# Performance work log

Hardware: AMD Instinct MI355X
Metric: run time of the kernel (lower is better)

## Reference

```python
import jax, jax.numpy as jnp
import numpy as np

B, IN, H, Z = 2048, 1024, 1024, 256


def setup_inputs() -> dict:
    key = jax.random.key(0)
    ks = jax.random.split(key, 17)
    s = 1.0 / np.sqrt(H)  # matches reset_parameters uniform(-stdv, stdv)
    u = lambda k, shape: jax.random.uniform(k, shape, minval=-s, maxval=s, dtype=jnp.float32)
    return {
        'src_x': jax.random.normal(ks[0], (B, IN), dtype=jnp.float32),
        'h': jax.random.normal(ks[1], (B, H), dtype=jnp.float32),
        'c': jax.random.normal(ks[2], (B, H), dtype=jnp.float32),
        'src_meta': jax.random.normal(ks[3], (B, Z), dtype=jnp.float32),
        'zh_w': u(ks[4], (4 * Z, Z)),
        'zh_b': u(ks[5], (4 * Z,)),
        'zx_w': u(ks[6], (4 * Z, Z)),
        'zx_b': u(ks[7], (4 * Z,)),
        'zb_w': u(ks[8], (4 * Z, Z)),
        'dh_w': u(ks[9], (4, H, Z)),
        'dx_w': u(ks[10], (4, H, Z)),
        'db_w': u(ks[11], (4, H, Z)),
        'db_b': u(ks[12], (4, H)),
        'w_h': u(ks[13], (4, H, H)),
        'w_x': u(ks[14], (4, H, IN)),
        'ln_w': u(ks[15], (4, H)),
        'ln_b': u(ks[16], (4, H)),
    }


def reference(src_x, h, c, src_meta, zh_w, zh_b, zx_w, zx_b, zb_w,
              dh_w, dx_w, db_w, db_b, w_h, w_x, ln_w, ln_b):
    b = src_x.shape[0]
    # hypernetwork projections, reshaped to [B, 4 gates, Z]
    zh = (src_meta @ zh_w.T + zh_b).reshape(b, 4, -1)
    zx = (src_meta @ zx_w.T + zx_b).reshape(b, 4, -1)
    zb = (src_meta @ zb_w.T).reshape(b, 4, -1)
    # per-gate scaling vectors d_h, d_x and bias d_b: [B, 4, H]
    d_h = jnp.einsum('bgz,ghz->bgh', zh, dh_w)
    d_x = jnp.einsum('bgz,ghz->bgh', zx, dx_w)
    d_b = jnp.einsum('bgz,ghz->bgh', zb, db_w) + db_b[None]
    # main LSTM matmuls: [B, 4, H]
    wh = jnp.einsum('ghj,bj->bgh', w_h, h)
    wx = jnp.einsum('ghj,bj->bgh', w_x, src_x)
    y = d_h * wh + d_x * wx + d_b
    # per-gate LayerNorm over hidden dim (eps = 1e-5, torch default)
    mu = jnp.mean(y, axis=-1, keepdims=True)
    var = jnp.var(y, axis=-1, keepdims=True)
    yn = (y - mu) * jax.lax.rsqrt(var + 1e-5) * ln_w[None] + ln_b[None]
    i, f, g, o = yn[:, 0], yn[:, 1], yn[:, 2], yn[:, 3]
    c_next = jax.nn.sigmoid(f) * c + jax.nn.sigmoid(i) * jnp.tanh(g)
    h_next = jax.nn.sigmoid(o) * jnp.tanh(c_next)
    return (h_next, c_next)
```

## Files before the change

### kernel.cpp

```cpp
#include <hip/hip_runtime.h>

typedef __attribute__((ext_vector_type(4))) float f32x4;
typedef __attribute__((ext_vector_type(16))) float f32x16;
typedef __attribute__((ext_vector_type(8))) short bf16x8;

#define DEVFN static __device__ __forceinline__

DEVFN unsigned short f2bf(float f) {
  union { float f; unsigned u; } x; x.f = f;
  unsigned r = x.u + 0x7fffu + ((x.u >> 16) & 1u);
  return (unsigned short)(r >> 16);
}
DEVFN float bf2f(unsigned short u) {
  union { unsigned u; float f; } x; x.u = ((unsigned)u) << 16;
  return x.f;
}

DEVFN void gload_lds16(const unsigned short* g, unsigned short* l) {
  __builtin_amdgcn_global_load_lds(
      (const __attribute__((address_space(1))) unsigned int*)g,
      (__attribute__((address_space(3))) unsigned int*)l, 16, 0, 0);
}

#define NSEG 8
struct SegTable {
  const float* src[NSEG];
  unsigned short* dst[NSEG];
  int chunks[NSEG];
};

__global__ __launch_bounds__(256) void cast_f32_bf16(SegTable st) {
  int c = blockIdx.x;
  int s = 0;
  while (c >= st.chunks[s]) { c -= st.chunks[s]; ++s; }
  const float* src = st.src[s] + (long)c * 4096;
  unsigned short* dst = st.dst[s] + (long)c * 4096;
  const int t = threadIdx.x;
#pragma unroll
  for (int i = 0; i < 4; ++i) {
    float4 v = *(const float4*)(src + t * 4 + i * 1024);
    ushort4 o;
    o.x = f2bf(v.x); o.y = f2bf(v.y); o.z = f2bf(v.z); o.w = f2bf(v.w);
    *(ushort4*)(dst + t * 4 + i * 1024) = o;
  }
}

__global__ __launch_bounds__(256) void tcast_z(
    const float* __restrict__ zh_w, const float* __restrict__ zx_w,
    const float* __restrict__ zb_w, unsigned short* __restrict__ WzT) {
  const int zz = blockIdx.z;
  const int t = zz >> 2, g = zz & 3;
  const float* src =
      (t == 0 ? zh_w : (t == 1 ? zx_w : zb_w)) + (long)g * 65536;
  unsigned short* dst = WzT + (long)zz * 65536;
  const int j0 = blockIdx.x * 64, k0 = blockIdx.y * 64;
  __shared__ float T[64][65];
  const int tid = threadIdx.x;
  const int jr = tid >> 2, kc = (tid & 3) * 16;
#pragma unroll
  for (int i = 0; i < 4; ++i) {
    float4 v = *(const float4*)(src + (long)(j0 + jr) * 256 + k0 + kc + i * 4);
    T[jr][kc + i * 4 + 0] = v.x;
    T[jr][kc + i * 4 + 1] = v.y;
    T[jr][kc + i * 4 + 2] = v.z;
    T[jr][kc + i * 4 + 3] = v.w;
  }
  __syncthreads();
  const int kr = tid >> 2, jc = (tid & 3) * 16;
  unsigned short tmp[16];
#pragma unroll
  for (int i = 0; i < 16; ++i) tmp[i] = f2bf(T[jc + i][kr]);
  *(bf16x8*)(dst + (long)(k0 + kr) * 256 + j0 + jc) = *(bf16x8*)&tmp[0];
  *(bf16x8*)(dst + (long)(k0 + kr) * 256 + j0 + jc + 8) = *(bf16x8*)&tmp[8];
}

__global__ __launch_bounds__(256) void fbias_kernel(
    const float* __restrict__ zh_b, const float* __restrict__ zx_b,
    const float* __restrict__ db_b, const float* __restrict__ dh_w,
    const float* __restrict__ dx_w, float* __restrict__ F) {
  if (blockIdx.x >= 128) {
    const int idx = (blockIdx.x - 128) * 1024 + threadIdx.x * 4;
    *(float4*)(F + 8192 + idx) = *(const float4*)(db_b + idx);
    return;
  }
  const int wgid = blockIdx.x * 4 + (threadIdx.x >> 6);
  const int lane = threadIdx.x & 63;
  const int t = wgid >> 8, g = (wgid >> 6) & 3, hbase = (wgid & 63) * 16;
  const float* zb = (t == 0 ? zh_b : zx_b) + g * 256;
  const float* dw = (t == 0 ? dh_w : dx_w) + (long)g * 262144;
  float4 zv = *(const float4*)(zb + lane * 4);
#pragma unroll
  for (int i = 0; i < 16; ++i) {
    const int h = hbase + i;
    float4 wv = *(const float4*)(dw + (long)h * 256 + lane * 4);
    float s = zv.x * wv.x + zv.y * wv.y + zv.z * wv.z + zv.w * wv.w;
#pragma unroll
    for (int off = 32; off; off >>= 1) s += __shfl_down(s, off);
    if (lane == 0) F[(t * 4 + g) * 1024 + h] = s;
  }
}

DEVFN void gemm128_body(const unsigned short* __restrict__ A,
                        const unsigned short* __restrict__ W,
                        unsigned short* __restrict__ C,
                        const float* __restrict__ bias,
                        int lda, int ldb, int ldc, int K,
                        int bx, int by,
                        unsigned short* As, unsigned short* Bs) {
  const int m0 = by * 128, n0 = bx * 128;
  const int tid = threadIdx.x;
  const int lane = tid & 63, wid = tid >> 6;
  const int wr = wid >> 1, wc = wid & 1;

  const int srow = tid >> 2, scol = (tid & 3) * 8;
  const unsigned short* Ag0 = A + (long)(m0 + srow) * lda + scol;
  const unsigned short* Ag1 = A + (long)(m0 + 64 + srow) * lda + scol;
  const unsigned short* Wg0 = W + (long)(n0 + srow) * ldb + scol;
  const unsigned short* Wg1 = W + (long)(n0 + 64 + srow) * ldb + scol;
  unsigned short* As0 = &As[tid * 8];
  unsigned short* As1 = &As[2048 + tid * 8];
  unsigned short* Bs0 = &Bs[tid * 8];
  unsigned short* Bs1 = &Bs[2048 + tid * 8];

  const int r = lane & 15, q = lane >> 4;

  f32x4 acc[4][4];
#pragma unroll
  for (int m = 0; m < 4; ++m)
#pragma unroll
    for (int n = 0; n < 4; ++n) acc[m][n] = (f32x4)0.f;

  for (int k0 = 0; k0 < K; k0 += 32) {
    gload_lds16(Ag0 + k0, As0);
    gload_lds16(Ag1 + k0, As1);
    gload_lds16(Wg0 + k0, Bs0);
    gload_lds16(Wg1 + k0, Bs1);
    __syncthreads();

    bf16x8 af[4], bfr[4];
#pragma unroll
    for (int m = 0; m < 4; ++m)
      af[m] = *(const bf16x8*)&As[(wr * 64 + m * 16 + r) * 32 + q * 8];
#pragma unroll
    for (int n = 0; n < 4; ++n)
      bfr[n] = *(const bf16x8*)&Bs[(wc * 64 + n * 16 + r) * 32 + q * 8];
#pragma unroll
    for (int m = 0; m < 4; ++m)
#pragma unroll
      for (int n = 0; n < 4; ++n)
        acc[m][n] = __builtin_amdgcn_mfma_f32_16x16x32_bf16(af[m], bfr[n],
                                                            acc[m][n], 0, 0, 0);
    __syncthreads();
  }

#pragma unroll
  for (int m = 0; m < 4; ++m) {
    const int row = m0 + wr * 64 + m * 16 + q * 4;
#pragma unroll
    for (int n = 0; n < 4; ++n) {
      const int col = n0 + wc * 64 + n * 16 + r;
      float bv = bias ? bias[col] : 0.f;
#pragma unroll
      for (int j = 0; j < 4; ++j) {
        float v = acc[m][n][j] + bv;
        C[(long)(row + j) * ldc + col] = f2bf(v);
      }
    }
  }
}

__global__ __launch_bounds__(256) void gemm_e(
    const unsigned short* __restrict__ Wd, const unsigned short* __restrict__ WzT,
    unsigned short* __restrict__ E) {
  __shared__ __align__(16) unsigned short As[4096];
  __shared__ __align__(16) unsigned short Bs[4096];
  const int zz = blockIdx.z;
  gemm128_body(Wd + (long)zz * 262144, WzT + (long)zz * 65536,
               E + (long)zz * 262144, nullptr,
               256, 256, 256, 256, blockIdx.x, blockIdx.y, As, Bs);
}

__global__ __launch_bounds__(256) void gemm_y(
    const unsigned short* __restrict__ meta_bf,
    const unsigned short* __restrict__ E,
    const unsigned short* __restrict__ whx,
    const float* __restrict__ F,
    unsigned short* __restrict__ Y) {
  __shared__ __align__(16) unsigned short As[4096];
  __shared__ __align__(16) unsigned short Bs[4096];
  const int g = blockIdx.z;
  const int m0 = blockIdx.y * 128, n0 = blockIdx.x * 128;
  const int tid = threadIdx.x;
  const int lane = tid & 63, wid = tid >> 6;
  const int wr = wid >> 1, wc = wid & 1;
  const int r = lane & 15, q = lane >> 4;
  const int srow = tid >> 2, scol = (tid & 3) * 8;

  const unsigned short* Ag0 = meta_bf + (long)(m0 + srow) * 256 + scol;
  const unsigned short* Ag1 = meta_bf + (long)(m0 + 64 + srow) * 256 + scol;
  unsigned short* As0 = &As[tid * 8];
  unsigned short* As1 = &As[2048 + tid * 8];
  unsigned short* Bs0 = &Bs[tid * 8];
  unsigned short* Bs1 = &Bs[2048 + tid * 8];

  f32x4 yacc[4][4];
#pragma unroll
  for (int m = 0; m < 4; ++m)
#pragma unroll
    for (int n = 0; n < 4; ++n) yacc[m][n] = (f32x4)0.f;

#pragma unroll 1
  for (int t = 0; t < 3; ++t) {
    const unsigned short* W = E + ((long)(t * 4 + g)) * 262144;
    const unsigned short* Wg0 = W + (long)(n0 + srow) * 256 + scol;
    const unsigned short* Wg1 = W + (long)(n0 + 64 + srow) * 256 + scol;

    f32x4 acc[4][4];
#pragma unroll
    for (int m = 0; m < 4; ++m)
#pragma unroll
      for (int n = 0; n < 4; ++n) acc[m][n] = (f32x4)0.f;

    for (int k0 = 0; k0 < 256; k0 += 32) {
      gload_lds16(Ag0 + k0, As0);
      gload_lds16(Ag1 + k0, As1);
      gload_lds16(Wg0 + k0, Bs0);
      gload_lds16(Wg1 + k0, Bs1);
      __syncthreads();

      bf16x8 af[4], bfr[4];
#pragma unroll
      for (int m = 0; m < 4; ++m)
        af[m] = *(const bf16x8*)&As[(wr * 64 + m * 16 + r) * 32 + q * 8];
#pragma unroll
      for (int n = 0; n < 4; ++n)
        bfr[n] = *(const bf16x8*)&Bs[(wc * 64 + n * 16 + r) * 32 + q * 8];
#pragma unroll
      for (int m = 0; m < 4; ++m)
#pragma unroll
        for (int n = 0; n < 4; ++n)
          acc[m][n] = __builtin_amdgcn_mfma_f32_16x16x32_bf16(
              af[m], bfr[n], acc[m][n], 0, 0, 0);
      __syncthreads();
    }

    if (t < 2) {
      const unsigned short* wsrc = whx + (long)t * 8388608;
#pragma unroll
      for (int n = 0; n < 4; ++n) {
        const int cl = wc * 64 + n * 16 + r;
        const float fv = F[(t * 4 + g) * 1024 + n0 + cl];
        const long colg = (long)g * 1024 + n0 + cl;
#pragma unroll
        for (int m = 0; m < 4; ++m) {
          const int row = m0 + wr * 64 + m * 16 + q * 4;
#pragma unroll
          for (int j = 0; j < 4; ++j) {
            const float wv = bf2f(wsrc[(long)(row + j) * 4096 + colg]);
            yacc[m][n][j] += (acc[m][n][j] + fv) * wv;
          }
        }
      }
    } else {
#pragma unroll
      for (int n = 0; n < 4; ++n) {
        const int cl = wc * 64 + n * 16 + r;
        const float fv = F[(8 + g) * 1024 + n0 + cl];
#pragma unroll
        for (int m = 0; m < 4; ++m)
#pragma unroll
          for (int j = 0; j < 4; ++j)
            yacc[m][n][j] += acc[m][n][j] + fv;
      }
    }
  }

#pragma unroll
  for (int m = 0; m < 4; ++m) {
    const int row = m0 + wr * 64 + m * 16 + q * 4;
#pragma unroll
    for (int n = 0; n < 4; ++n) {
      const long colg = (long)g * 1024 + n0 + wc * 64 + n * 16 + r;
#pragma unroll
      for (int j = 0; j < 4; ++j)
        Y[(long)(row + j) * 4096 + colg] = f2bf(yacc[m][n][j]);
    }
  }
}

__global__ __launch_bounds__(512, 2) void gemm256_whx(
    const unsigned short* __restrict__ Aall,
    const unsigned short* __restrict__ Ball,
    unsigned short* __restrict__ Call) {
  __shared__ __align__(16) unsigned short As[2][2][8192];
  __shared__ __align__(16) unsigned short Bs[2][2][8192];

  const int bid = blockIdx.x;
  const int swz = (bid & 7) * 32 + (bid >> 3);
  const int z = swz >> 7;
  const int rr = swz & 127;
  const int sb = rr >> 5, wq = rr & 31;
  const int my = (sb & 1) * 4 + (wq >> 3);
  const int nx = (sb >> 1) * 8 + (wq & 7);

  const unsigned short* Ag = Aall + (long)z * 2097152 + (long)my * 262144;
  const unsigned short* Bg = Ball + (long)z * 4194304 + (long)nx * 262144;
  unsigned short* Cg = Call + (long)z * 8388608 + (long)my * 1048576 + nx * 256;

  const int tid = threadIdx.x;
  const int lane = tid & 63, wid = tid >> 6;
  const int wm = wid >> 2, wn = wid & 3;
  const int l31 = lane & 31, l5 = lane >> 5;
  const int sw = l31 & 7;

  const int srow = tid >> 3, sslot = tid & 7;
  const int gcol = (sslot ^ (srow & 7)) * 8;
  const unsigned short* AgS = Ag + (long)srow * 1024 + gcol;
  const unsigned short* BgS = Bg + (long)srow * 1024 + gcol;

  auto stageA = [&](int buf, int half, int kt) {
    const unsigned short* s = AgS + half * 131072 + kt * 64;
    unsigned short* d = &As[buf][half][tid * 8];
    gload_lds16(s, d);
    gload_lds16(s + 65536, d + 4096);
  };
  auto stageB = [&](int buf, int half, int kt) {
    const unsigned short* s = BgS + half * 131072 + kt * 64;
    unsigned short* d = &Bs[buf][half][tid * 8];
    gload_lds16(s, d);
    gload_lds16(s + 65536, d + 4096);
  };

  int koff[4];
#pragma unroll
  for (int ks = 0; ks < 4; ++ks) koff[ks] = ((ks * 2 + l5) ^ sw) * 8;

  const int bhalf = wn >> 1;
  int brow[2];
#pragma unroll
  for (int nt = 0; nt < 2; ++nt) brow[nt] = ((wn & 1) * 64 + nt * 32 + l31) * 64;
  int arow[4];
#pragma unroll
  for (int mt = 0; mt < 4; ++mt) arow[mt] = (mt * 32 + l31) * 64;

  f32x16 acc[4][2];
#pragma unroll
  for (int m = 0; m < 4; ++m)
#pragma unroll
    for (int n = 0; n < 2; ++n) acc[m][n] = (f32x16)0.f;

  stageA(0, 0, 0); stageB(0, 0, 0); stageA(0, 1, 0); stageB(0, 1, 0);
  stageA(1, 0, 1); stageB(1, 0, 1);
  asm volatile("s_waitcnt vmcnt(4)" ::: "memory");
  __builtin_amdgcn_s_barrier();

#pragma unroll 2
  for (int T = 0; T < 16; ++T) {
    const int buf = T & 1, nb = buf ^ 1;

    if (T < 15) { stageA(nb, 1, T + 1); stageB(nb, 1, T + 1); }

    bf16x8 bfg[2][4], af[2][4];
    const unsigned short* Ab = &As[buf][wm][0];
    {
      const unsigned short* Bb = &Bs[buf][bhalf][0];
#pragma unroll
      for (int nt = 0; nt < 2; ++nt)
#pragma unroll
        for (int ks = 0; ks < 4; ++ks)
          bfg[nt][ks] = *(const bf16x8*)(Bb + brow[nt] + koff[ks]);
#pragma unroll
      for (int m2 = 0; m2 < 2; ++m2)
#pragma unroll
        for (int ks = 0; ks < 4; ++ks)
          af[m2][ks] = *(const bf16x8*)(Ab + arow[m2] + koff[ks]);
    }

    __builtin_amdgcn_s_setprio(1);
#pragma unroll
    for (int m2 = 0; m2 < 2; ++m2)
#pragma unroll
      for (int nt = 0; nt < 2; ++nt)
#pragma unroll
        for (int ks = 0; ks < 4; ++ks)
          acc[m2][nt] = __builtin_amdgcn_mfma_f32_32x32x16_bf16(
              af[m2][ks], bfg[nt][ks], acc[m2][nt], 0, 0, 0);
    __builtin_amdgcn_s_setprio(0);

#pragma unroll
    for (int m2 = 0; m2 < 2; ++m2)
#pragma unroll
      for (int ks = 0; ks < 4; ++ks)
        af[m2][ks] = *(const bf16x8*)(Ab + arow[2 + m2] + koff[ks]);

    asm volatile("s_waitcnt lgkmcnt(0)" ::: "memory");
    __builtin_amdgcn_sched_barrier(0);
    __builtin_amdgcn_s_barrier();

    if (T < 14) { stageA(buf, 0, T + 2); stageB(buf, 0, T + 2); }

    __builtin_amdgcn_s_setprio(1);
#pragma unroll
    for (int m2 = 0; m2 < 2; ++m2)
#pragma unroll
      for (int nt = 0; nt < 2; ++nt)
#pragma unroll
        for (int ks = 0; ks < 4; ++ks)
          acc[2 + m2][nt] = __builtin_amdgcn_mfma_f32_32x32x16_bf16(
              af[m2][ks], bfg[nt][ks], acc[2 + m2][nt], 0, 0, 0);
    __builtin_amdgcn_s_setprio(0);

    if (T < 14) {
      asm volatile("s_waitcnt vmcnt(4)" ::: "memory");
      __builtin_amdgcn_s_barrier();
    } else if (T == 14) {
      asm volatile("s_waitcnt vmcnt(0)" ::: "memory");
      __builtin_amdgcn_s_barrier();
    }
  }

#pragma unroll
  for (int mt = 0; mt < 4; ++mt) {
#pragma unroll
    for (int nt = 0; nt < 2; ++nt) {
      const int rb = wm * 128 + mt * 32 + 4 * l5;
      const int cb = wn * 64 + nt * 32 + l31;
#pragma unroll
      for (int reg = 0; reg < 16; ++reg) {
        const int row = rb + (reg & 3) + 8 * (reg >> 2);
        Cg[(long)row * 4096 + cb] = f2bf(acc[mt][nt][reg]);
      }
    }
  }
}

DEVFN void ld4bf(const unsigned short* p, float* o) {
  ushort4 v = *(const ushort4*)p;
  o[0] = bf2f(v.x); o[1] = bf2f(v.y); o[2] = bf2f(v.z); o[3] = bf2f(v.w);
}

__global__ __launch_bounds__(256) void epilogue2(
    const unsigned short* __restrict__ Y,
    const float* __restrict__ c_in,
    const float* __restrict__ ln_w, const float* __restrict__ ln_b,
    float* __restrict__ out) {
  const long b = blockIdx.x;
  const int t = threadIdx.x;
  const int lane = t & 63, wid = t >> 6;

  __shared__ float redS[4][4], redQ[4][4];
  float y[4][4];

#pragma unroll
  for (int g = 0; g < 4; ++g) {
    ld4bf(Y + b * 4096 + g * 1024 + t * 4, y[g]);
    float s = 0.f, sq = 0.f;
#pragma unroll
    for (int j = 0; j < 4; ++j) { s += y[g][j]; sq += y[g][j] * y[g][j]; }
#pragma unroll
    for (int off = 32; off; off >>= 1) {
      s += __shfl_down(s, off);
      sq += __shfl_down(sq, off);
    }
    if (lane == 0) { redS[g][wid] = s; redQ[g][wid] = sq; }
  }
  __syncthreads();

  float yn[4][4];
#pragma unroll
  for (int g = 0; g < 4; ++g) {
    float S = redS[g][0] + redS[g][1] + redS[g][2] + redS[g][3];
    float SQ = redQ[g][0] + redQ[g][1] + redQ[g][2] + redQ[g][3];
    float mu = S * (1.f / 1024.f);
    float var = SQ * (1.f / 1024.f) - mu * mu;
    float rs = rsqrtf(var + 1e-5f);
    const int base = g * 1024 + t * 4;
    float4 lw = *(const float4*)(ln_w + base);
    float4 lb = *(const float4*)(ln_b + base);
    yn[g][0] = (y[g][0] - mu) * rs * lw.x + lb.x;
    yn[g][1] = (y[g][1] - mu) * rs * lw.y + lb.y;
    yn[g][2] = (y[g][2] - mu) * rs * lw.z + lb.z;
    yn[g][3] = (y[g][3] - mu) * rs * lw.w + lb.w;
  }

  float4 cp = *(const float4*)(c_in + b * 1024 + t * 4);
  float cin[4] = {cp.x, cp.y, cp.z, cp.w};
  float hn[4], cn[4];
#pragma unroll
  for (int j = 0; j < 4; ++j) {
    float ii = yn[0][j], ff = yn[1][j], gg = yn[2][j], oo = yn[3][j];
    float si = 1.f / (1.f + expf(-ii));
    float sf = 1.f / (1.f + expf(-ff));
    float so = 1.f / (1.f + expf(-oo));
    float cnj = sf * cin[j] + si * tanhf(gg);
    cn[j] = cnj;
    hn[j] = so * tanhf(cnj);
  }
  float4 ho = {hn[0], hn[1], hn[2], hn[3]};
  float4 co = {cn[0], cn[1], cn[2], cn[3]};
  *(float4*)(out + b * 1024 + t * 4) = ho;
  *(float4*)(out + 2097152L + b * 1024 + t * 4) = co;
}

extern "C" void kernel_launch(void* const* d_in, const int* in_sizes, int n_in,
                              void* d_out, int out_size, void* d_ws,
                              size_t ws_size, hipStream_t stream) {
  const float* src_x = (const float*)d_in[0];
  const float* h_in  = (const float*)d_in[1];
  const float* c_in  = (const float*)d_in[2];
  const float* meta  = (const float*)d_in[3];
  const float* zh_w  = (const float*)d_in[4];
  const float* zh_b  = (const float*)d_in[5];
  const float* zx_w  = (const float*)d_in[6];
  const float* zx_b  = (const float*)d_in[7];
  const float* zb_w  = (const float*)d_in[8];
  const float* dh_w  = (const float*)d_in[9];
  const float* dx_w  = (const float*)d_in[10];
  const float* db_w  = (const float*)d_in[11];
  const float* db_b  = (const float*)d_in[12];
  const float* w_h   = (const float*)d_in[13];
  const float* w_x   = (const float*)d_in[14];
  const float* ln_w  = (const float*)d_in[15];
  const float* ln_b  = (const float*)d_in[16];

  char* ws = (char*)d_ws;
  unsigned short* h_bf    = (unsigned short*)(ws + 0);
  unsigned short* x_bf    = (unsigned short*)(ws + 4194304);
  unsigned short* meta_bf = (unsigned short*)(ws + 8388608);
  unsigned short* Wh      = (unsigned short*)(ws + 9437184);
  unsigned short* Wx      = (unsigned short*)(ws + 17825792);
  unsigned short* Wd      = (unsigned short*)(ws + 26214400);
  unsigned short* WzT     = (unsigned short*)(ws + 32505856);
  unsigned short* E       = (unsigned short*)(ws + 34078720);
  float*          F       = (float*)(ws + 40370176);
  unsigned short* Ybuf    = (unsigned short*)(ws + 40419328);
  unsigned short* whx     = (unsigned short*)(ws + 57196544);
  if (ws_size < 90750976) return;

  SegTable st;
  int i = 0, total = 0;
  auto add = [&](const float* s, unsigned short* d, int n) {
    st.src[i] = s; st.dst[i] = d; st.chunks[i] = n / 4096;
    total += n / 4096; ++i;
  };
  add(h_in, h_bf, 2048 * 1024);
  add(src_x, x_bf, 2048 * 1024);
  add(meta, meta_bf, 2048 * 256);
  add(w_h, Wh, 4096 * 1024);
  add(w_x, Wx, 4096 * 1024);
  add(dh_w, Wd, 4 * 1024 * 256);
  add(dx_w, Wd + 1048576, 4 * 1024 * 256);
  add(db_w, Wd + 2097152, 4 * 1024 * 256);
  cast_f32_bf16<<<total, 256, 0, stream>>>(st);

  tcast_z<<<dim3(4, 4, 12), 256, 0, stream>>>(zh_w, zx_w, zb_w, WzT);
  fbias_kernel<<<132, 256, 0, stream>>>(zh_b, zx_b, db_b, dh_w, dx_w, F);

  gemm_e<<<dim3(2, 8, 12), 256, 0, stream>>>(Wd, WzT, E);

  gemm256_whx<<<256, 512, 0, stream>>>(h_bf, Wh, whx);

  gemm_y<<<dim3(8, 16, 4), 256, 0, stream>>>(meta_bf, E, whx, F, Ybuf);

  epilogue2<<<2048, 256, 0, stream>>>(Ybuf, c_in, ln_w, ln_b, (float*)d_out);
}
```

Before: 128.3 us.

## Merge prep kernels and stage gemm_y epilogue through LDS for coalesced access

Folds the three preprocessing kernels (cast, transpose-cast, bias) into one launch that dispatches on block index, removing two kernel launches. In gemm_y, each gate accumulator is biased, packed to bf16 and written to an enlarged shared buffer. Threads then re-read it in row-major 8-wide vectors, so the whx reads and final Y stores become coalesced 16-byte accesses instead of scattered 2-byte ones. This costs extra syncthreads, more LDS per block and an extra bf16 rounding of the intermediate before multiplying.

```diff
diff --git a/kernel.cpp b/kernel.cpp
--- a/kernel.cpp
+++ b/kernel.cpp
@@ -29,62 +29,67 @@
   int chunks[NSEG];
 };
 
-__global__ __launch_bounds__(256) void cast_f32_bf16(SegTable st) {
-  int c = blockIdx.x;
-  int s = 0;
-  while (c >= st.chunks[s]) { c -= st.chunks[s]; ++s; }
-  const float* src = st.src[s] + (long)c * 4096;
-  unsigned short* dst = st.dst[s] + (long)c * 4096;
-  const int t = threadIdx.x;
-#pragma unroll
-  for (int i = 0; i < 4; ++i) {
-    float4 v = *(const float4*)(src + t * 4 + i * 1024);
-    ushort4 o;
-    o.x = f2bf(v.x); o.y = f2bf(v.y); o.z = f2bf(v.z); o.w = f2bf(v.w);
-    *(ushort4*)(dst + t * 4 + i * 1024) = o;
-  }
-}
-
-__global__ __launch_bounds__(256) void tcast_z(
+__global__ __launch_bounds__(256) void prep_kernel(
+    SegTable st, int castChunks,
     const float* __restrict__ zh_w, const float* __restrict__ zx_w,
-    const float* __restrict__ zb_w, unsigned short* __restrict__ WzT) {
-  const int zz = blockIdx.z;
-  const int t = zz >> 2, g = zz & 3;
-  const float* src =
-      (t == 0 ? zh_w : (t == 1 ? zx_w : zb_w)) + (long)g * 65536;
-  unsigned short* dst = WzT + (long)zz * 65536;
-  const int j0 = blockIdx.x * 64, k0 = blockIdx.y * 64;
-  __shared__ float T[64][65];
-  const int tid = threadIdx.x;
-  const int jr = tid >> 2, kc = (tid & 3) * 16;
-#pragma unroll
-  for (int i = 0; i < 4; ++i) {
-    float4 v = *(const float4*)(src + (long)(j0 + jr) * 256 + k0 + kc + i * 4);
-    T[jr][kc + i * 4 + 0] = v.x;
-    T[jr][kc + i * 4 + 1] = v.y;
-    T[jr][kc + i * 4 + 2] = v.z;
-    T[jr][kc + i * 4 + 3] = v.w;
-  }
-  __syncthreads();
-  const int kr = tid >> 2, jc = (tid & 3) * 16;
-  unsigned short tmp[16];
-#pragma unroll
-  for (int i = 0; i < 16; ++i) tmp[i] = f2bf(T[jc + i][kr]);
-  *(bf16x8*)(dst + (long)(k0 + kr) * 256 + j0 + jc) = *(bf16x8*)&tmp[0];
-  *(bf16x8*)(dst + (long)(k0 + kr) * 256 + j0 + jc + 8) = *(bf16x8*)&tmp[8];
-}
-
-__global__ __launch_bounds__(256) void fbias_kernel(
+    const float* __restrict__ zb_w, unsigned short* __restrict__ WzT,
     const float* __restrict__ zh_b, const float* __restrict__ zx_b,
     const float* __restrict__ db_b, const float* __restrict__ dh_w,
     const float* __restrict__ dx_w, float* __restrict__ F) {
-  if (blockIdx.x >= 128) {
-    const int idx = (blockIdx.x - 128) * 1024 + threadIdx.x * 4;
+  __shared__ float T[64][65];
+  const int tid = threadIdx.x;
+  int b = blockIdx.x;
+
+  if (b < castChunks) {
+    int c = b, s = 0;
+    while (c >= st.chunks[s]) { c -= st.chunks[s]; ++s; }
+    const float* src = st.src[s] + (long)c * 4096;
+    unsigned short* dst = st.dst[s] + (long)c * 4096;
+#pragma unroll
+    for (int i = 0; i < 4; ++i) {
+      float4 v = *(const float4*)(src + tid * 4 + i * 1024);
+      ushort4 o;
+      o.x = f2bf(v.x); o.y = f2bf(v.y); o.z = f2bf(v.z); o.w = f2bf(v.w);
+      *(ushort4*)(dst + tid * 4 + i * 1024) = o;
+    }
+    return;
+  }
+  b -= castChunks;
+
+  if (b < 192) {
+    const int zz = b >> 4, rem = b & 15;
+    const int t = zz >> 2, g = zz & 3;
+    const float* src =
+        (t == 0 ? zh_w : (t == 1 ? zx_w : zb_w)) + (long)g * 65536;
+    unsigned short* dst = WzT + (long)zz * 65536;
+    const int j0 = (rem & 3) * 64, k0 = (rem >> 2) * 64;
+    const int jr = tid >> 2, kc = (tid & 3) * 16;
+#pragma unroll
+    for (int i = 0; i < 4; ++i) {
+      float4 v = *(const float4*)(src + (long)(j0 + jr) * 256 + k0 + kc + i * 4);
+      T[jr][kc + i * 4 + 0] = v.x;
+      T[jr][kc + i * 4 + 1] = v.y;
+      T[jr][kc + i * 4 + 2] = v.z;
+      T[jr][kc + i * 4 + 3] = v.w;
+    }
+    __syncthreads();
+    const int kr = tid >> 2, jc = (tid & 3) * 16;
+    unsigned short tmp[16];
+#pragma unroll
+    for (int i = 0; i < 16; ++i) tmp[i] = f2bf(T[jc + i][kr]);
+    *(bf16x8*)(dst + (long)(k0 + kr) * 256 + j0 + jc) = *(bf16x8*)&tmp[0];
+    *(bf16x8*)(dst + (long)(k0 + kr) * 256 + j0 + jc + 8) = *(bf16x8*)&tmp[8];
+    return;
+  }
+  b -= 192;
+
+  if (b >= 128) {
+    const int idx = (b - 128) * 1024 + tid * 4;
     *(float4*)(F + 8192 + idx) = *(const float4*)(db_b + idx);
     return;
   }
-  const int wgid = blockIdx.x * 4 + (threadIdx.x >> 6);
-  const int lane = threadIdx.x & 63;
+  const int wgid = b * 4 + (tid >> 6);
+  const int lane = tid & 63;
   const int t = wgid >> 8, g = (wgid >> 6) & 3, hbase = (wgid & 63) * 16;
   const float* zb = (t == 0 ? zh_b : zx_b) + g * 256;
   const float* dw = (t == 0 ? dh_w : dx_w) + (long)g * 262144;
@@ -186,8 +191,10 @@
     const unsigned short* __restrict__ whx,
     const float* __restrict__ F,
     unsigned short* __restrict__ Y) {
-  __shared__ __align__(16) unsigned short As[4096];
-  __shared__ __align__(16) unsigned short Bs[4096];
+  __shared__ __align__(16) unsigned short S[16384];
+  unsigned short* As = S;
+  unsigned short* Bs = S + 4096;
+
   const int g = blockIdx.z;
   const int m0 = blockIdx.y * 128, n0 = blockIdx.x * 128;
   const int tid = threadIdx.x;
@@ -195,6 +202,7 @@
   const int wr = wid >> 1, wc = wid & 1;
   const int r = lane & 15, q = lane >> 4;
   const int srow = tid >> 2, scol = (tid & 3) * 8;
+  const int lrow = tid >> 4, lcol = (tid & 15) * 8;
 
   const unsigned short* Ag0 = meta_bf + (long)(m0 + srow) * 256 + scol;
   const unsigned short* Ag1 = meta_bf + (long)(m0 + 64 + srow) * 256 + scol;
@@ -203,15 +211,16 @@
   unsigned short* Bs0 = &Bs[tid * 8];
   unsigned short* Bs1 = &Bs[2048 + tid * 8];
 
-  f32x4 yacc[4][4];
-#pragma unroll
-  for (int m = 0; m < 4; ++m)
-#pragma unroll
-    for (int n = 0; n < 4; ++n) yacc[m][n] = (f32x4)0.f;
+  float yacc[8][8];
+#pragma unroll
+  for (int i = 0; i < 8; ++i)
+#pragma unroll
+    for (int e = 0; e < 8; ++e) yacc[i][e] = 0.f;
 
 #pragma unroll 1
   for (int t = 0; t < 3; ++t) {
-    const unsigned short* W = E + ((long)(t * 4 + g)) * 262144;
+    const int zz = t * 4 + g;
+    const unsigned short* W = E + (long)zz * 262144;
     const unsigned short* Wg0 = W + (long)(n0 + srow) * 256 + scol;
     const unsigned short* Wg1 = W + (long)(n0 + 64 + srow) * 256 + scol;
 
@@ -244,47 +253,51 @@
       __syncthreads();
     }
 
+    const float* Fz = F + (long)zz * 1024 + n0;
+#pragma unroll
+    for (int n = 0; n < 4; ++n) {
+      const int col = wc * 64 + n * 16 + r;
+      const float fv = Fz[col];
+#pragma unroll
+      for (int m = 0; m < 4; ++m) {
+        const int rowb = wr * 64 + m * 16 + q * 4;
+#pragma unroll
+        for (int j = 0; j < 4; ++j)
+          S[(rowb + j) * 128 + col] = f2bf(acc[m][n][j] + fv);
+      }
+    }
+    __syncthreads();
+
     if (t < 2) {
-      const unsigned short* wsrc = whx + (long)t * 8388608;
-#pragma unroll
-      for (int n = 0; n < 4; ++n) {
-        const int cl = wc * 64 + n * 16 + r;
-        const float fv = F[(t * 4 + g) * 1024 + n0 + cl];
-        const long colg = (long)g * 1024 + n0 + cl;
-#pragma unroll
-        for (int m = 0; m < 4; ++m) {
-          const int row = m0 + wr * 64 + m * 16 + q * 4;
-#pragma unroll
-          for (int j = 0; j < 4; ++j) {
-            const float wv = bf2f(wsrc[(long)(row + j) * 4096 + colg]);
-            yacc[m][n][j] += (acc[m][n][j] + fv) * wv;
-          }
-        }
+      const unsigned short* wsrc =
+          whx + (long)t * 8388608 + (long)m0 * 4096 + g * 1024 + n0;
+#pragma unroll
+      for (int i = 0; i < 8; ++i) {
+        bf16x8 dv = *(const bf16x8*)&S[(i * 16 + lrow) * 128 + lcol];
+        bf16x8 wv = *(const bf16x8*)(wsrc + (long)(i * 16 + lrow) * 4096 + lcol);
+#pragma unroll
+        for (int e = 0; e < 8; ++e)
+          yacc[i][e] += bf2f((unsigned short)dv[e]) * bf2f((unsigned short)wv[e]);
       }
     } else {
 #pragma unroll
-      for (int n = 0; n < 4; ++n) {
-        const int cl = wc * 64 + n * 16 + r;
-        const float fv = F[(8 + g) * 1024 + n0 + cl];
-#pragma unroll
-        for (int m = 0; m < 4; ++m)
-#pragma unroll
-          for (int j = 0; j < 4; ++j)
-            yacc[m][n][j] += acc[m][n][j] + fv;
+      for (int i = 0; i < 8; ++i) {
+        bf16x8 dv = *(const bf16x8*)&S[(i * 16 + lrow) * 128 + lcol];
+#pragma unroll
+        for (int e = 0; e < 8; ++e)
+          yacc[i][e] += bf2f((unsigned short)dv[e]);
       }
     }
-  }
-
-#pragma unroll
-  for (int m = 0; m < 4; ++m) {
-    const int row = m0 + wr * 64 + m * 16 + q * 4;
-#pragma unroll
-    for (int n = 0; n < 4; ++n) {
-      const long colg = (long)g * 1024 + n0 + wc * 64 + n * 16 + r;
-#pragma unroll
-      for (int j = 0; j < 4; ++j)
-        Y[(long)(row + j) * 4096 + colg] = f2bf(yacc[m][n][j]);
-    }
+    __syncthreads();
+  }
+
+  unsigned short* Yt = Y + (long)m0 * 4096 + g * 1024 + n0;
+#pragma unroll
+  for (int i = 0; i < 8; ++i) {
+    unsigned short tmp[8];
+#pragma unroll
+    for (int e = 0; e < 8; ++e) tmp[e] = f2bf(yacc[i][e]);
+    *(bf16x8*)(Yt + (long)(i * 16 + lrow) * 4096 + lcol) = *(bf16x8*)&tmp[0];
   }
 }
 
@@ -551,10 +564,9 @@
   add(dh_w, Wd, 4 * 1024 * 256);
   add(dx_w, Wd + 1048576, 4 * 1024 * 256);
   add(db_w, Wd + 2097152, 4 * 1024 * 256);
-  cast_f32_bf16<<<total, 256, 0, stream>>>(st);
-
-  tcast_z<<<dim3(4, 4, 12), 256, 0, stream>>>(zh_w, zx_w, zb_w, WzT);
-  fbias_kernel<<<132, 256, 0, stream>>>(zh_b, zx_b, db_b, dh_w, dx_w, F);
+
+  prep_kernel<<<total + 192 + 132, 256, 0, stream>>>(
+      st, total, zh_w, zx_w, zb_w, WzT, zh_b, zx_b, db_b, dh_w, dx_w, F);
 
   gemm_e<<<dim3(2, 8, 12), 256, 0, stream>>>(Wd, WzT, E);
 
```

Result: no change. 130.1 us (+1.4%).
